# Optimization experiments

Measured on AMD Instinct MI355X. Metric: run time of the kernel, lower is better.

The kernel has to match this reference:

```python
import jax, jax.numpy as jnp
import numpy as np

K = 8192
D = 512
BETA = 0.25


def setup_inputs() -> dict:
    key = jax.random.key(0)
    k_z, k_cb = jax.random.split(key)
    z = jax.random.normal(k_z, (8, 4096, D), dtype=jnp.float32)
    codebook = jax.random.normal(k_cb, (K, D), dtype=jnp.float32)
    return {"z": z, "codebook": codebook}


def reference(z, codebook):
    B, Q, Din = z.shape
    flat = z.reshape(-1, Din)                      # (N, D)
    x2 = jnp.sum(flat * flat, axis=1, keepdims=True)   # (N, 1)
    e2 = jnp.sum(codebook * codebook, axis=1)          # (K,)
    xe = flat @ codebook.T                             # (N, K)
    distances = x2 - 2.0 * xe + e2[None, :]
    indices = jnp.argmin(distances, axis=1)            # (N,)
    z_q = codebook[indices].reshape(B, Q, Din)

    codebook_loss = jnp.mean((z_q - jax.lax.stop_gradient(z)) ** 2)
    commitment_loss = jnp.mean((z - jax.lax.stop_gradient(z_q)) ** 2)
    vq_loss = codebook_loss + BETA * commitment_loss
    z_q_ste = z + jax.lax.stop_gradient(z_q - z)

    # perplexity from one-hot usage counts of this batch
    N = flat.shape[0]
    counts = jnp.zeros((codebook.shape[0],), dtype=jnp.float32).at[indices].add(1.0)
    probs = counts / jnp.asarray(N, dtype=jnp.float32)
    perplexity = jnp.exp(-jnp.sum(probs * jnp.log(probs + 1e-10)))

    return z_q_ste, vq_loss, indices.reshape(B, Q), perplexity
```

## Files before the change

kernel.cpp:

```cpp
#include <hip/hip_runtime.h>
#include <hip/hip_bf16.h>

#define K_CODES 8192
#define DIM     512
#define N_VEC   32768
#define MARGIN  0.35f
#define MARGIN2 0.02f

typedef __attribute__((ext_vector_type(8))) short   short8;
typedef __attribute__((ext_vector_type(8))) unsigned short ushort8;
typedef __attribute__((ext_vector_type(4))) float   float4x;

__device__ inline void gl_lds16(const void* g, void* l) {
    __builtin_amdgcn_global_load_lds(
        (const __attribute__((address_space(1))) unsigned int*)g,
        (__attribute__((address_space(3))) unsigned int*)l, 16, 0, 0);
}

__device__ inline unsigned short f2bf(float f, float* back) {
    unsigned int u = __float_as_uint(f);
    unsigned int r = (u + 0x7FFFu + ((u >> 16) & 1u)) >> 16;
    *back = __uint_as_float(r << 16);
    return (unsigned short)r;
}

__global__ __launch_bounds__(256) void vq_prep(
    const float* __restrict__ z, const float* __restrict__ cb,
    float* __restrict__ x2, float* __restrict__ hne2,
    unsigned short* __restrict__ zh, unsigned short* __restrict__ zl,
    unsigned short* __restrict__ ch, unsigned short* __restrict__ cl) {
    int wave = threadIdx.x >> 6;
    int lane = threadIdx.x & 63;
    int row  = blockIdx.x * 4 + wave;
    bool isZ = row < N_VEC;
    int lr = isZ ? row : row - N_VEC;
    const float* src = isZ ? z + (size_t)row * DIM : cb + (size_t)lr * DIM;

    const float4* s4 = (const float4*)src;
    float4 v0 = s4[lane * 2];
    float4 v1 = s4[lane * 2 + 1];
    float f[8] = {v0.x, v0.y, v0.z, v0.w, v1.x, v1.y, v1.z, v1.w};

    float s = 0.0f;
    ushort8 h8, l8;
#pragma unroll
    for (int i = 0; i < 8; ++i) {
        s += f[i] * f[i];
        float back, dummy;
        h8[i] = f2bf(f[i], &back);
        l8[i] = f2bf(f[i] - back, &dummy);
    }
    ((ushort8*)(isZ ? zh : ch))[(size_t)lr * 64 + lane] = h8;
    ((ushort8*)(isZ ? zl : cl))[(size_t)lr * 64 + lane] = l8;

#pragma unroll
    for (int off = 32; off >= 1; off >>= 1) s += __shfl_xor(s, off, 64);
    if (lane == 0) {
        if (isZ) x2[lr] = s;
        else     hne2[lr] = -0.5f * s;
    }
}

__global__ __launch_bounds__(256, 2) void vq_gemm(
    const unsigned short* __restrict__ zh, const unsigned short* __restrict__ ch,
    const float* __restrict__ hne2,
    float* __restrict__ pG, int* __restrict__ pN, float* __restrict__ pG2) {
    __shared__ short8 AsC[1024];
    __shared__ short8 BsC[2048];

    const int tid  = threadIdx.x;
    const int w    = tid >> 6;
    const int lane = tid & 63;
    const int wM   = w & 1;
    const int wN   = w >> 1;
    const int rowBase   = blockIdx.x * 128;
    const int half      = blockIdx.y;
    const int codeBase0 = half * 4096;

    const int low3 = lane & 7, m15 = lane & 15, hi4 = lane >> 4;

    unsigned aOff[4];
#pragma unroll
    for (int i = 0; i < 4; ++i) {
        int cell = (w * 4 + i) * 64 + lane;
        int r = cell >> 3, qs = cell & 7, q = qs ^ (r & 7);
        aOff[i] = ((unsigned)(rowBase + r) * DIM + q * 8) * 2;
    }
    unsigned bOff[8];
#pragma unroll
    for (int i = 0; i < 8; ++i) {
        int cell = (w * 8 + i) * 64 + lane;
        int c = cell >> 3, qs = cell & 7, q = qs ^ (c & 7);
        bOff[i] = ((unsigned)c * DIM + q * 8) * 2;
    }

    int rIdx[4], cIdx[8];
#pragma unroll
    for (int mf = 0; mf < 4; ++mf) rIdx[mf] = (wM * 64 + mf * 16 + m15) * 8;
#pragma unroll
    for (int nf = 0; nf < 8; ++nf) cIdx[nf] = (wN * 128 + nf * 16 + m15) * 8;

    float g1[4][4], g2[4][4];
    int   n1[4][4];
#pragma unroll
    for (int mf = 0; mf < 4; ++mf)
#pragma unroll
        for (int rg = 0; rg < 4; ++rg) {
            g1[mf][rg] = -3.4e38f; g2[mf][rg] = -3.4e38f; n1[mf][rg] = 0;
        }

    const char* pA = (const char*)zh;
    for (int ct = 0; ct < 16; ++ct) {
        const int codeBase = codeBase0 + ct * 256;
        const char* pB = (const char*)ch + (size_t)codeBase * (DIM * 2);
        float4x acc[4][8];
#pragma unroll
        for (int mf = 0; mf < 4; ++mf)
#pragma unroll
            for (int nf = 0; nf < 8; ++nf) acc[mf][nf] = (float4x){0.f, 0.f, 0.f, 0.f};

        for (int dc = 0; dc < DIM; dc += 64) {
            const int dc2 = dc * 2;
            __syncthreads();
#pragma unroll
            for (int i = 0; i < 4; ++i)
                gl_lds16(pA + aOff[i] + dc2, &AsC[(w * 4 + i) * 64]);
#pragma unroll
            for (int i = 0; i < 8; ++i)
                gl_lds16(pB + bOff[i] + dc2, &BsC[(w * 8 + i) * 64]);
            __syncthreads();

#pragma unroll
            for (int ks = 0; ks < 2; ++ks) {
                const int qx = (ks * 4 + hi4) ^ low3;
                short8 a[4];
#pragma unroll
                for (int mf = 0; mf < 4; ++mf) a[mf] = AsC[rIdx[mf] + qx];
#pragma unroll
                for (int nf = 0; nf < 8; ++nf) {
                    short8 b = BsC[cIdx[nf] + qx];
#pragma unroll
                    for (int mf = 0; mf < 4; ++mf)
                        acc[mf][nf] = __builtin_amdgcn_mfma_f32_16x16x32_bf16(
                            a[mf], b, acc[mf][nf], 0, 0, 0);
                }
            }
        }

#pragma unroll
        for (int nf = 0; nf < 8; ++nf) {
            int nb = codeBase + wN * 128 + nf * 16 + m15;
            float hv = hne2[nb];
#pragma unroll
            for (int mf = 0; mf < 4; ++mf) {
#pragma unroll
                for (int rg = 0; rg < 4; ++rg) {
                    float g = acc[mf][nf][rg] + hv;
                    if (g > g1[mf][rg]) {
                        g2[mf][rg] = g1[mf][rg];
                        g1[mf][rg] = g; n1[mf][rg] = nb;
                    } else {
                        g2[mf][rg] = fmaxf(g2[mf][rg], g);
                    }
                }
            }
        }
    }

#pragma unroll
    for (int mf = 0; mf < 4; ++mf)
#pragma unroll
        for (int rg = 0; rg < 4; ++rg) {
            float a1 = g1[mf][rg], a2 = g2[mf][rg];
            int   an = n1[mf][rg];
#pragma unroll
            for (int off = 1; off <= 8; off <<= 1) {
                float b1 = __shfl_xor(a1, off, 64);
                int   bn = __shfl_xor(an, off, 64);
                float b2 = __shfl_xor(a2, off, 64);
                if (b1 > a1 || (b1 == a1 && bn < an)) {
                    a2 = fmaxf(a1, b2); a1 = b1; an = bn;
                } else {
                    a2 = fmaxf(a2, b1);
                }
            }
            if (m15 == 0) {
                int row  = rowBase + wM * 64 + mf * 16 + hi4 * 4 + rg;
                int slot = half * 2 + wN;
                pG [slot * N_VEC + row] = a1;
                pN [slot * N_VEC + row] = an;
                pG2[slot * N_VEC + row] = a2;
            }
        }
}

__global__ __launch_bounds__(256) void vq_scan(
    float* __restrict__ pG, const int* __restrict__ pN,
    const float* __restrict__ pG2,
    int* __restrict__ provIdx, int* __restrict__ flags,
    unsigned long long* __restrict__ keys,
    int* __restrict__ rescueRows, int* __restrict__ rescueCnt) {
    int r = blockIdx.x * 256 + threadIdx.x;
    float g1 = pG[r], g2 = pG2[r];
    int   n1 = pN[r];
#pragma unroll
    for (int s = 1; s < 4; ++s) {
        float a1 = pG [s * N_VEC + r];
        int   an = pN [s * N_VEC + r];
        float a2 = pG2[s * N_VEC + r];
        if (a1 > g1 || (a1 == g1 && an < n1)) {
            g2 = fmaxf(g1, a2); g1 = a1; n1 = an;
        } else {
            g2 = fmaxf(g2, a1);
        }
    }
    provIdx[r] = n1;
    pG[r] = g1;
    int fl = (g1 - g2 < MARGIN) ? 1 : 0;
    flags[r] = fl;
    if (fl) {
        keys[r] = ~0ull;
        int p = atomicAdd(rescueCnt, 1);
        rescueRows[p] = r;
    }
}

__global__ __launch_bounds__(256, 2) void vq_mid(
    const unsigned short* __restrict__ zh, const unsigned short* __restrict__ zl,
    const unsigned short* __restrict__ ch, const unsigned short* __restrict__ cl,
    const float* __restrict__ hne2,
    const int* __restrict__ rescueRows, const int* __restrict__ rescueCnt,
    float* __restrict__ pGm, int* __restrict__ pNm, float* __restrict__ pG2m) {
    __shared__ short8 AsC[512];
    __shared__ short8 BsC[2048];
    __shared__ int rowOf[64];

    const int tid  = threadIdx.x;
    const int w    = tid >> 6;
    const int lane = tid & 63;
    const int wM   = w & 1;
    const int wN   = w >> 1;
    const int cnt  = *rescueCnt;
    const int codeBase0 = blockIdx.y * 1024;

    const int low3 = lane & 7, m15 = lane & 15, hi4 = lane >> 4;

    unsigned bOff[8];
#pragma unroll
    for (int i = 0; i < 8; ++i) {
        int cell = (w * 8 + i) * 64 + lane;
        int c = cell >> 3, qs = cell & 7, q = qs ^ (c & 7);
        bOff[i] = ((unsigned)c * DIM + q * 8) * 2;
    }
    int aCellR[2], aCellQ[2];
#pragma unroll
    for (int i = 0; i < 2; ++i) {
        int cell = (w * 2 + i) * 64 + lane;
        aCellR[i] = cell >> 3;
        aCellQ[i] = (cell & 7) ^ (aCellR[i] & 7);
    }

    int rIdx[2], cIdx[8];
#pragma unroll
    for (int mf = 0; mf < 2; ++mf) rIdx[mf] = (wM * 32 + mf * 16 + m15) * 8;
#pragma unroll
    for (int nf = 0; nf < 8; ++nf) cIdx[nf] = (wN * 128 + nf * 16 + m15) * 8;

    for (int rt = blockIdx.x; rt * 64 < cnt; rt += gridDim.x) {
        __syncthreads();
        if (tid < 64) rowOf[tid] = rescueRows[rt * 64 + tid];
        __syncthreads();

        unsigned aOff[2];
#pragma unroll
        for (int i = 0; i < 2; ++i)
            aOff[i] = ((unsigned)rowOf[aCellR[i]] * DIM + aCellQ[i] * 8) * 2;

        float g1[2][4], g2[2][4];
        int   n1[2][4];
#pragma unroll
        for (int mf = 0; mf < 2; ++mf)
#pragma unroll
            for (int rg = 0; rg < 4; ++rg) {
                g1[mf][rg] = -3.4e38f; g2[mf][rg] = -3.4e38f; n1[mf][rg] = 0;
            }

        for (int ct = 0; ct < 4; ++ct) {
            const int codeBase = codeBase0 + ct * 256;
            float4x acc[2][8];
#pragma unroll
            for (int mf = 0; mf < 2; ++mf)
#pragma unroll
                for (int nf = 0; nf < 8; ++nf) acc[mf][nf] = (float4x){0.f, 0.f, 0.f, 0.f};

#pragma unroll
            for (int pass = 0; pass < 3; ++pass) {
                const char* pA = (const char*)(pass == 1 ? zl : zh);
                const char* pB = (const char*)(pass == 2 ? cl : ch)
                                 + (size_t)codeBase * (DIM * 2);
                for (int dc = 0; dc < DIM; dc += 64) {
                    const int dc2 = dc * 2;
                    __syncthreads();
#pragma unroll
                    for (int i = 0; i < 2; ++i)
                        gl_lds16(pA + aOff[i] + dc2, &AsC[(w * 2 + i) * 64]);
#pragma unroll
                    for (int i = 0; i < 8; ++i)
                        gl_lds16(pB + bOff[i] + dc2, &BsC[(w * 8 + i) * 64]);
                    __syncthreads();

#pragma unroll
                    for (int ks = 0; ks < 2; ++ks) {
                        const int qx = (ks * 4 + hi4) ^ low3;
                        short8 a[2];
#pragma unroll
                        for (int mf = 0; mf < 2; ++mf) a[mf] = AsC[rIdx[mf] + qx];
#pragma unroll
                        for (int nf = 0; nf < 8; ++nf) {
                            short8 b = BsC[cIdx[nf] + qx];
#pragma unroll
                            for (int mf = 0; mf < 2; ++mf)
                                acc[mf][nf] = __builtin_amdgcn_mfma_f32_16x16x32_bf16(
                                    a[mf], b, acc[mf][nf], 0, 0, 0);
                        }
                    }
                }
            }

#pragma unroll
            for (int nf = 0; nf < 8; ++nf) {
                int nb = codeBase + wN * 128 + nf * 16 + m15;
                float hv = hne2[nb];
#pragma unroll
                for (int mf = 0; mf < 2; ++mf) {
#pragma unroll
                    for (int rg = 0; rg < 4; ++rg) {
                        float g = acc[mf][nf][rg] + hv;
                        if (g > g1[mf][rg]) {
                            g2[mf][rg] = g1[mf][rg];
                            g1[mf][rg] = g; n1[mf][rg] = nb;
                        } else {
                            g2[mf][rg] = fmaxf(g2[mf][rg], g);
                        }
                    }
                }
            }
        }

#pragma unroll
        for (int mf = 0; mf < 2; ++mf)
#pragma unroll
            for (int rg = 0; rg < 4; ++rg) {
                float a1 = g1[mf][rg], a2 = g2[mf][rg];
                int   an = n1[mf][rg];
#pragma unroll
                for (int off = 1; off <= 8; off <<= 1) {
                    float b1 = __shfl_xor(a1, off, 64);
                    int   bn = __shfl_xor(an, off, 64);
                    float b2 = __shfl_xor(a2, off, 64);
                    if (b1 > a1 || (b1 == a1 && bn < an)) {
                        a2 = fmaxf(a1, b2); a1 = b1; an = bn;
                    } else {
                        a2 = fmaxf(a2, b1);
                    }
                }
                if (m15 == 0) {
                    int sPos = rt * 64 + wM * 32 + mf * 16 + hi4 * 4 + rg;
                    int slot = blockIdx.y * 2 + wN;
                    pGm [slot * N_VEC + sPos] = a1;
                    pNm [slot * N_VEC + sPos] = an;
                    pG2m[slot * N_VEC + sPos] = a2;
                }
            }
    }
}

__global__ __launch_bounds__(256) void vq_scan2(
    const float* __restrict__ pGm, const int* __restrict__ pNm,
    const float* __restrict__ pG2m,
    const int* __restrict__ rescueRows, const int* __restrict__ rescueCnt,
    unsigned long long* __restrict__ keys,
    int* __restrict__ rescueRows2, int* __restrict__ rescueCnt2) {
    int s = blockIdx.x * 256 + threadIdx.x;
    if (s >= *rescueCnt) return;
    float g1 = pGm[s], g2 = pG2m[s];
    int   n1 = pNm[s];
#pragma unroll
    for (int k = 1; k < 16; ++k) {
        float a1 = pGm [k * N_VEC + s];
        int   an = pNm [k * N_VEC + s];
        float a2 = pG2m[k * N_VEC + s];
        if (a1 > g1 || (a1 == g1 && an < n1)) {
            g2 = fmaxf(g1, a2); g1 = a1; n1 = an;
        } else {
            g2 = fmaxf(g2, a1);
        }
    }
    int row = rescueRows[s];
    if (g1 - g2 < MARGIN2) {
        keys[row] = ~0ull;
        int p = atomicAdd(rescueCnt2, 1);
        rescueRows2[p] = row;
    } else {
        keys[row] = ((unsigned long long)__float_as_uint(-g1) << 32) |
                    (unsigned long long)(unsigned)n1;
    }
}

#define RBM 64
#define RBK 256
#define RBD 32

__global__ __launch_bounds__(256, 2) void vq_exact(
    const float* __restrict__ z, const float* __restrict__ cb,
    const float* __restrict__ hne2,
    const int* __restrict__ rescueRows2, const int* __restrict__ rescueCnt2,
    unsigned long long* __restrict__ keys) {
    __shared__ float As[RBD][RBM];
    __shared__ float Bs[RBD][RBK];
    __shared__ int   rowOf[RBM];

    const int tid = threadIdx.x;
    const int tx  = tid & 31;
    const int ty  = tid >> 5;
    const int cnt = *rescueCnt2;
    const int codeBase0 = blockIdx.y * 512;
    const int sw = (tx & 8) ? 4 : 0;
    const int sRow = tid >> 2;
    const int sQ   = tid & 3;

    for (int rt = blockIdx.x; rt * RBM < cnt; rt += gridDim.x) {
        const int slotBase = rt * RBM;
        __syncthreads();
        if (tid < RBM) rowOf[tid] = rescueRows2[slotBase + tid];
        __syncthreads();

        float best[8];
        int   bidx[8];
#pragma unroll
        for (int i = 0; i < 8; ++i) { best[i] = 3.4e38f; bidx[i] = K_CODES; }

        for (int kt = 0; kt < 2; ++kt) {
            const int codeBase = codeBase0 + kt * RBK;
            float acc[8][8];
#pragma unroll
            for (int i = 0; i < 8; ++i)
#pragma unroll
                for (int j = 0; j < 8; ++j) acc[i][j] = 0.0f;

            for (int dc = 0; dc < DIM; dc += RBD) {
                __syncthreads();
                {
                    const float* srcA = z + (size_t)rowOf[sRow] * DIM + dc + sQ * 8;
                    float4 va0 = ((const float4*)srcA)[0];
                    float4 va1 = ((const float4*)srcA)[1];
                    int c0 = sQ * 8;
                    As[c0 + 0][sRow] = va0.x; As[c0 + 1][sRow] = va0.y;
                    As[c0 + 2][sRow] = va0.z; As[c0 + 3][sRow] = va0.w;
                    As[c0 + 4][sRow] = va1.x; As[c0 + 5][sRow] = va1.y;
                    As[c0 + 6][sRow] = va1.z; As[c0 + 7][sRow] = va1.w;
                }
                {
                    const float4* srcB = (const float4*)(cb + (size_t)(codeBase + tid) * DIM + dc);
#pragma unroll
                    for (int j = 0; j < 8; ++j) {
                        float4 v = srcB[j];
                        Bs[j * 4 + 0][tid] = v.x; Bs[j * 4 + 1][tid] = v.y;
                        Bs[j * 4 + 2][tid] = v.z; Bs[j * 4 + 3][tid] = v.w;
                    }
                }
                __syncthreads();

#pragma unroll
                for (int d = 0; d < RBD; ++d) {
                    float a[8], b[8];
                    *(float4*)&a[0] = *(const float4*)&As[d][ty * 8];
                    *(float4*)&a[4] = *(const float4*)&As[d][ty * 8 + 4];
                    *(float4*)&b[0] = *(const float4*)&Bs[d][tx * 8 + sw];
                    *(float4*)&b[4] = *(const float4*)&Bs[d][tx * 8 + (sw ^ 4)];
#pragma unroll
                    for (int i = 0; i < 8; ++i)
#pragma unroll
                        for (int j = 0; j < 8; ++j) acc[i][j] += a[i] * b[j];
                }
            }

#pragma unroll
            for (int j = 0; j < 8; ++j) {
                int code = codeBase + tx * 8 + ((j < 4) ? (sw + j) : ((sw ^ 4) + j - 4));
                float ev = -hne2[code];
#pragma unroll
                for (int i = 0; i < 8; ++i) {
                    float kv = ev - acc[i][j];
                    if (kv < best[i] || (kv == best[i] && code < bidx[i])) {
                        best[i] = kv;
                        bidx[i] = code;
                    }
                }
            }
        }

#pragma unroll
        for (int off = 16; off >= 1; off >>= 1) {
#pragma unroll
            for (int i = 0; i < 8; ++i) {
                float od = __shfl_xor(best[i], off, 64);
                int   oi = __shfl_xor(bidx[i], off, 64);
                if (od < best[i] || (od == best[i] && oi < bidx[i])) {
                    best[i] = od;
                    bidx[i] = oi;
                }
            }
        }

        if (tx == 0) {
#pragma unroll
            for (int i = 0; i < 8; ++i) {
                int slot = slotBase + ty * 8 + i;
                if (slot < cnt) {
                    unsigned long long key =
                        ((unsigned long long)__float_as_uint(best[i]) << 32) |
                        (unsigned long long)(unsigned)bidx[i];
                    atomicMin(&keys[rowOf[ty * 8 + i]], key);
                }
            }
        }
    }
}

__global__ __launch_bounds__(256) void vq_final(
    const float* __restrict__ gBest, const int* __restrict__ provIdx,
    const int* __restrict__ flags, const unsigned long long* __restrict__ keys,
    const float* __restrict__ x2, const float* __restrict__ cb,
    float* __restrict__ zq, float* __restrict__ idxf,
    float* __restrict__ counts, float* __restrict__ lossAcc) {
    __shared__ int   sIdx[256];
    __shared__ float wsum[4];
    const int tid = threadIdx.x;
    const int r   = blockIdx.x * 256 + tid;

    int n; float dist;
    if (flags[r]) {
        unsigned long long k = keys[r];
        n = (int)(unsigned)(k & 0xffffffffu);
        float kv = __uint_as_float((unsigned)(k >> 32));
        dist = x2[r] + 2.0f * kv;
    } else {
        n = provIdx[r];
        dist = x2[r] - 2.0f * gBest[r];
    }
    sIdx[tid] = n;
    idxf[r]   = (float)n;
    atomicAdd(&counts[n], 1.0f);

    float ls = dist;
#pragma unroll
    for (int off = 32; off >= 1; off >>= 1) ls += __shfl_xor(ls, off, 64);
    if ((tid & 63) == 0) wsum[tid >> 6] = ls;
    __syncthreads();
    if (tid == 0) atomicAdd(lossAcc, wsum[0] + wsum[1] + wsum[2] + wsum[3]);

    const float4* cb4 = (const float4*)cb;
    float4* zq4 = (float4*)(zq + (size_t)blockIdx.x * 256 * DIM);
    for (int t = tid; t < 256 * (DIM / 4); t += 256) {
        int row = t >> 7, f4 = t & 127;
        zq4[(size_t)row * 128 + f4] = cb4[(size_t)sIdx[row] * 128 + f4];
    }
}

__global__ __launch_bounds__(256) void vq_finalize(const float* __restrict__ counts,
                                                   const float* __restrict__ lossAcc,
                                                   float* __restrict__ out_loss,
                                                   float* __restrict__ out_perp) {
    __shared__ float wsum[4];
    int tid = threadIdx.x;
    float s = 0.0f;
    for (int i = tid; i < K_CODES; i += 256) {
        float p = counts[i] * (1.0f / (float)N_VEC);
        s += p * logf(p + 1e-10f);
    }
#pragma unroll
    for (int off = 32; off >= 1; off >>= 1) s += __shfl_xor(s, off, 64);
    if ((tid & 63) == 0) wsum[tid >> 6] = s;
    __syncthreads();
    if (tid == 0) {
        *out_perp = expf(-(wsum[0] + wsum[1] + wsum[2] + wsum[3]));
        *out_loss = 1.25f * lossAcc[0] / (float)(N_VEC * DIM);
    }
}

extern "C" void kernel_launch(void* const* d_in, const int* in_sizes, int n_in,
                              void* d_out, int out_size, void* d_ws, size_t ws_size,
                              hipStream_t stream) {
    (void)in_sizes; (void)n_in; (void)out_size; (void)ws_size;
    const float* z  = (const float*)d_in[0];
    const float* cb = (const float*)d_in[1];

    char* ws = (char*)d_ws;
    float* x2         = (float*)(ws + 0);
    float* hne2       = (float*)(ws + 131072);
    float* counts     = (float*)(ws + 163840);
    float* lossAcc    = (float*)(ws + 196608);
    int*   rescueCnt  = (int*)  (ws + 196612);
    int*   rescueCnt2 = (int*)  (ws + 196616);
    int*   provIdx    = (int*)  (ws + 262144);
    int*   flags      = (int*)  (ws + 393216);
    unsigned long long* keys = (unsigned long long*)(ws + 524288);
    int*   rescueRows  = (int*)(ws + 786432);
    int*   rescueRows2 = (int*)(ws + 917504);
    float* pG         = (float*)(ws + 1048576);
    int*   pN         = (int*)  (ws + 1572864);
    float* pG2        = (float*)(ws + 2097152);
    float* pGm        = (float*)(ws + 2621440);
    int*   pNm        = (int*)  (ws + 4718592);
    float* pG2m       = (float*)(ws + 6815744);
    unsigned short* zh = (unsigned short*)(ws + 8912896);
    unsigned short* zl = (unsigned short*)(ws + 42467328);
    unsigned short* ch = (unsigned short*)(ws + 76021760);
    unsigned short* cl = (unsigned short*)(ws + 84410368);

    float* out      = (float*)d_out;
    float* zq       = out;
    float* out_loss = out + 16777216;
    float* idxf     = out + 16777217;
    float* out_perp = out + 16777217 + 32768;

    hipMemsetAsync(counts, 0, 32768 + 12, stream);
    hipMemsetAsync(rescueRows, 0, 262144, stream);
    vq_prep<<<(N_VEC + K_CODES) / 4, 256, 0, stream>>>(z, cb, x2, hne2, zh, zl, ch, cl);
    dim3 grid(N_VEC / 128, 2);
    vq_gemm<<<grid, 256, 0, stream>>>(zh, ch, hne2, pG, pN, pG2);
    vq_scan<<<N_VEC / 256, 256, 0, stream>>>(pG, pN, pG2, provIdx, flags, keys,
                                             rescueRows, rescueCnt);
    dim3 mgrid(32, 8);
    vq_mid<<<mgrid, 256, 0, stream>>>(zh, zl, ch, cl, hne2, rescueRows, rescueCnt,
                                      pGm, pNm, pG2m);
    vq_scan2<<<N_VEC / 256, 256, 0, stream>>>(pGm, pNm, pG2m, rescueRows, rescueCnt,
                                              keys, rescueRows2, rescueCnt2);
    dim3 egrid(8, 16);
    vq_exact<<<egrid, 256, 0, stream>>>(z, cb, hne2, rescueRows2, rescueCnt2, keys);
    vq_final<<<N_VEC / 256, 256, 0, stream>>>(pG, provIdx, flags, keys, x2, cb,
                                              zq, idxf, counts, lossAcc);
    vq_finalize<<<1, 256, 0, stream>>>(counts, lossAcc, out_loss, out_perp);
}
```

Baseline: 728.0 us.

## Retile rescue GEMM to 128-row by 256-code tiles and cap rescue count

```diff
diff --git a/kernel.cpp b/kernel.cpp
--- a/kernel.cpp
+++ b/kernel.cpp
@@ -6,6 +6,7 @@
 #define N_VEC   32768
 #define MARGIN  0.35f
 #define MARGIN2 0.02f
+#define MAXC    8192
 
 typedef __attribute__((ext_vector_type(8))) short   short8;
 typedef __attribute__((ext_vector_type(8))) unsigned short ushort8;
@@ -199,7 +200,8 @@
     const float* __restrict__ pG2,
     int* __restrict__ provIdx, int* __restrict__ flags,
     unsigned long long* __restrict__ keys,
-    int* __restrict__ rescueRows, int* __restrict__ rescueCnt) {
+    int* __restrict__ rescueRows, int* __restrict__ rescueCnt,
+    int* __restrict__ rescueRows2, int* __restrict__ rescueCnt2) {
     int r = blockIdx.x * 256 + threadIdx.x;
     float g1 = pG[r], g2 = pG2[r];
     int   n1 = pN[r];
@@ -221,7 +223,12 @@
     if (fl) {
         keys[r] = ~0ull;
         int p = atomicAdd(rescueCnt, 1);
-        rescueRows[p] = r;
+        if (p < MAXC) {
+            rescueRows[p] = r;
+        } else {
+            int q = atomicAdd(rescueCnt2, 1);
+            rescueRows2[q] = r;
+        }
     }
 }
 
@@ -231,124 +238,119 @@
     const float* __restrict__ hne2,
     const int* __restrict__ rescueRows, const int* __restrict__ rescueCnt,
     float* __restrict__ pGm, int* __restrict__ pNm, float* __restrict__ pG2m) {
-    __shared__ short8 AsC[512];
+    __shared__ short8 AsC[1024];
     __shared__ short8 BsC[2048];
-    __shared__ int rowOf[64];
+    __shared__ int rowOf[128];
 
     const int tid  = threadIdx.x;
     const int w    = tid >> 6;
     const int lane = tid & 63;
     const int wM   = w & 1;
     const int wN   = w >> 1;
-    const int cnt  = *rescueCnt;
-    const int codeBase0 = blockIdx.y * 1024;
+    int cnt = *rescueCnt; if (cnt > MAXC) cnt = MAXC;
+    const int rowTiles = (cnt + 127) >> 7;
+    const int codeBase = blockIdx.y * 256;
 
     const int low3 = lane & 7, m15 = lane & 15, hi4 = lane >> 4;
 
+    int aCellR[4], aCellQ[4];
+#pragma unroll
+    for (int i = 0; i < 4; ++i) {
+        int cell = (w * 4 + i) * 64 + lane;
+        aCellR[i] = cell >> 3;
+        aCellQ[i] = (cell & 7) ^ (aCellR[i] & 7);
+    }
     unsigned bOff[8];
 #pragma unroll
     for (int i = 0; i < 8; ++i) {
         int cell = (w * 8 + i) * 64 + lane;
         int c = cell >> 3, qs = cell & 7, q = qs ^ (c & 7);
-        bOff[i] = ((unsigned)c * DIM + q * 8) * 2;
-    }
-    int aCellR[2], aCellQ[2];
-#pragma unroll
-    for (int i = 0; i < 2; ++i) {
-        int cell = (w * 2 + i) * 64 + lane;
-        aCellR[i] = cell >> 3;
-        aCellQ[i] = (cell & 7) ^ (aCellR[i] & 7);
-    }
-
-    int rIdx[2], cIdx[8];
-#pragma unroll
-    for (int mf = 0; mf < 2; ++mf) rIdx[mf] = (wM * 32 + mf * 16 + m15) * 8;
+        bOff[i] = ((unsigned)(codeBase + c) * DIM + q * 8) * 2;
+    }
+
+    int rIdx[4], cIdx[8];
+#pragma unroll
+    for (int mf = 0; mf < 4; ++mf) rIdx[mf] = (wM * 64 + mf * 16 + m15) * 8;
 #pragma unroll
     for (int nf = 0; nf < 8; ++nf) cIdx[nf] = (wN * 128 + nf * 16 + m15) * 8;
 
-    for (int rt = blockIdx.x; rt * 64 < cnt; rt += gridDim.x) {
+    for (int rt = blockIdx.x; rt < rowTiles; rt += gridDim.x) {
         __syncthreads();
-        if (tid < 64) rowOf[tid] = rescueRows[rt * 64 + tid];
+        if (tid < 128) rowOf[tid] = rescueRows[rt * 128 + tid];
         __syncthreads();
 
-        unsigned aOff[2];
-#pragma unroll
-        for (int i = 0; i < 2; ++i)
+        unsigned aOff[4];
+#pragma unroll
+        for (int i = 0; i < 4; ++i)
             aOff[i] = ((unsigned)rowOf[aCellR[i]] * DIM + aCellQ[i] * 8) * 2;
 
-        float g1[2][4], g2[2][4];
-        int   n1[2][4];
-#pragma unroll
-        for (int mf = 0; mf < 2; ++mf)
+        float4x acc[4][8];
+#pragma unroll
+        for (int mf = 0; mf < 4; ++mf)
+#pragma unroll
+            for (int nf = 0; nf < 8; ++nf) acc[mf][nf] = (float4x){0.f, 0.f, 0.f, 0.f};
+
+#pragma unroll
+        for (int pass = 0; pass < 3; ++pass) {
+            const char* pA = (const char*)(pass == 1 ? zl : zh);
+            const char* pB = (const char*)(pass == 2 ? cl : ch);
+            for (int dc = 0; dc < DIM; dc += 64) {
+                const int dc2 = dc * 2;
+                __syncthreads();
+#pragma unroll
+                for (int i = 0; i < 4; ++i)
+                    gl_lds16(pA + aOff[i] + dc2, &AsC[(w * 4 + i) * 64]);
+#pragma unroll
+                for (int i = 0; i < 8; ++i)
+                    gl_lds16(pB + bOff[i] + dc2, &BsC[(w * 8 + i) * 64]);
+                __syncthreads();
+
+#pragma unroll
+                for (int ks = 0; ks < 2; ++ks) {
+                    const int qx = (ks * 4 + hi4) ^ low3;
+                    short8 a[4];
+#pragma unroll
+                    for (int mf = 0; mf < 4; ++mf) a[mf] = AsC[rIdx[mf] + qx];
+#pragma unroll
+                    for (int nf = 0; nf < 8; ++nf) {
+                        short8 b = BsC[cIdx[nf] + qx];
+#pragma unroll
+                        for (int mf = 0; mf < 4; ++mf)
+                            acc[mf][nf] = __builtin_amdgcn_mfma_f32_16x16x32_bf16(
+                                a[mf], b, acc[mf][nf], 0, 0, 0);
+                    }
+                }
+            }
+        }
+
+        float g1[4][4], g2[4][4];
+        int   n1[4][4];
+#pragma unroll
+        for (int mf = 0; mf < 4; ++mf)
 #pragma unroll
             for (int rg = 0; rg < 4; ++rg) {
                 g1[mf][rg] = -3.4e38f; g2[mf][rg] = -3.4e38f; n1[mf][rg] = 0;
             }
-
-        for (int ct = 0; ct < 4; ++ct) {
-            const int codeBase = codeBase0 + ct * 256;
-            float4x acc[2][8];
-#pragma unroll
-            for (int mf = 0; mf < 2; ++mf)
-#pragma unroll
-                for (int nf = 0; nf < 8; ++nf) acc[mf][nf] = (float4x){0.f, 0.f, 0.f, 0.f};
-
-#pragma unroll
-            for (int pass = 0; pass < 3; ++pass) {
-                const char* pA = (const char*)(pass == 1 ? zl : zh);
-                const char* pB = (const char*)(pass == 2 ? cl : ch)
-                                 + (size_t)codeBase * (DIM * 2);
-                for (int dc = 0; dc < DIM; dc += 64) {
-                    const int dc2 = dc * 2;
-                    __syncthreads();
-#pragma unroll
-                    for (int i = 0; i < 2; ++i)
-                        gl_lds16(pA + aOff[i] + dc2, &AsC[(w * 2 + i) * 64]);
-#pragma unroll
-                    for (int i = 0; i < 8; ++i)
-                        gl_lds16(pB + bOff[i] + dc2, &BsC[(w * 8 + i) * 64]);
-                    __syncthreads();
-
-#pragma unroll
-                    for (int ks = 0; ks < 2; ++ks) {
-                        const int qx = (ks * 4 + hi4) ^ low3;
-                        short8 a[2];
-#pragma unroll
-                        for (int mf = 0; mf < 2; ++mf) a[mf] = AsC[rIdx[mf] + qx];
-#pragma unroll
-                        for (int nf = 0; nf < 8; ++nf) {
-                            short8 b = BsC[cIdx[nf] + qx];
-#pragma unroll
-                            for (int mf = 0; mf < 2; ++mf)
-                                acc[mf][nf] = __builtin_amdgcn_mfma_f32_16x16x32_bf16(
-                                    a[mf], b, acc[mf][nf], 0, 0, 0);
-                        }
+#pragma unroll
+        for (int nf = 0; nf < 8; ++nf) {
+            int nb = codeBase + wN * 128 + nf * 16 + m15;
+            float hv = hne2[nb];
+#pragma unroll
+            for (int mf = 0; mf < 4; ++mf) {
+#pragma unroll
+                for (int rg = 0; rg < 4; ++rg) {
+                    float g = acc[mf][nf][rg] + hv;
+                    if (g > g1[mf][rg]) {
+                        g2[mf][rg] = g1[mf][rg];
+                        g1[mf][rg] = g; n1[mf][rg] = nb;
+                    } else {
+                        g2[mf][rg] = fmaxf(g2[mf][rg], g);
                     }
                 }
             }
-
-#pragma unroll
-            for (int nf = 0; nf < 8; ++nf) {
-                int nb = codeBase + wN * 128 + nf * 16 + m15;
-                float hv = hne2[nb];
-#pragma unroll
-                for (int mf = 0; mf < 2; ++mf) {
-#pragma unroll
-                    for (int rg = 0; rg < 4; ++rg) {
-                        float g = acc[mf][nf][rg] + hv;
-                        if (g > g1[mf][rg]) {
-                            g2[mf][rg] = g1[mf][rg];
-                            g1[mf][rg] = g; n1[mf][rg] = nb;
-                        } else {
-                            g2[mf][rg] = fmaxf(g2[mf][rg], g);
-                        }
-                    }
-                }
-            }
-        }
-
-#pragma unroll
-        for (int mf = 0; mf < 2; ++mf)
+        }
+#pragma unroll
+        for (int mf = 0; mf < 4; ++mf)
 #pragma unroll
             for (int rg = 0; rg < 4; ++rg) {
                 float a1 = g1[mf][rg], a2 = g2[mf][rg];
@@ -365,11 +367,11 @@
                     }
                 }
                 if (m15 == 0) {
-                    int sPos = rt * 64 + wM * 32 + mf * 16 + hi4 * 4 + rg;
+                    int sPos = rt * 128 + wM * 64 + mf * 16 + hi4 * 4 + rg;
                     int slot = blockIdx.y * 2 + wN;
-                    pGm [slot * N_VEC + sPos] = a1;
-                    pNm [slot * N_VEC + sPos] = an;
-                    pG2m[slot * N_VEC + sPos] = a2;
+                    pGm [slot * MAXC + sPos] = a1;
+                    pNm [slot * MAXC + sPos] = an;
+                    pG2m[slot * MAXC + sPos] = a2;
                 }
             }
     }
@@ -382,14 +384,15 @@
     unsigned long long* __restrict__ keys,
     int* __restrict__ rescueRows2, int* __restrict__ rescueCnt2) {
     int s = blockIdx.x * 256 + threadIdx.x;
-    if (s >= *rescueCnt) return;
+    int cnt = *rescueCnt; if (cnt > MAXC) cnt = MAXC;
+    if (s >= cnt) return;
     float g1 = pGm[s], g2 = pG2m[s];
     int   n1 = pNm[s];
-#pragma unroll
-    for (int k = 1; k < 16; ++k) {
-        float a1 = pGm [k * N_VEC + s];
-        int   an = pNm [k * N_VEC + s];
-        float a2 = pG2m[k * N_VEC + s];
+#pragma unroll 8
+    for (int k = 1; k < 64; ++k) {
+        float a1 = pGm [k * MAXC + s];
+        int   an = pNm [k * MAXC + s];
+        float a2 = pG2m[k * MAXC + s];
         if (a1 > g1 || (a1 == g1 && an < n1)) {
             g2 = fmaxf(g1, a2); g1 = a1; n1 = an;
         } else {
@@ -631,12 +634,13 @@
     dim3 grid(N_VEC / 128, 2);
     vq_gemm<<<grid, 256, 0, stream>>>(zh, ch, hne2, pG, pN, pG2);
     vq_scan<<<N_VEC / 256, 256, 0, stream>>>(pG, pN, pG2, provIdx, flags, keys,
-                                             rescueRows, rescueCnt);
-    dim3 mgrid(32, 8);
+                                             rescueRows, rescueCnt,
+                                             rescueRows2, rescueCnt2);
+    dim3 mgrid(16, 32);
     vq_mid<<<mgrid, 256, 0, stream>>>(zh, zl, ch, cl, hne2, rescueRows, rescueCnt,
                                       pGm, pNm, pG2m);
-    vq_scan2<<<N_VEC / 256, 256, 0, stream>>>(pGm, pNm, pG2m, rescueRows, rescueCnt,
-                                              keys, rescueRows2, rescueCnt2);
+    vq_scan2<<<MAXC / 256, 256, 0, stream>>>(pGm, pNm, pG2m, rescueRows, rescueCnt,
+                                             keys, rescueRows2, rescueCnt2);
     dim3 egrid(8, 16);
     vq_exact<<<egrid, 256, 0, stream>>>(z, cb, hne2, rescueRows2, rescueCnt2, keys);
     vq_final<<<N_VEC / 256, 256, 0, stream>>>(pG, provIdx, flags, keys, x2, cb,
```

New measurement: 686.8 us. 1.06x faster.

## Flatten rescue GEMM work into row-tile by code-strip units with capped rescue list

Applied to the files above, without the earlier changes.

```diff
diff --git a/kernel.cpp b/kernel.cpp
--- a/kernel.cpp
+++ b/kernel.cpp
@@ -6,6 +6,7 @@
 #define N_VEC   32768
 #define MARGIN  0.35f
 #define MARGIN2 0.02f
+#define MAXC    8192
 
 typedef __attribute__((ext_vector_type(8))) short   short8;
 typedef __attribute__((ext_vector_type(8))) unsigned short ushort8;
@@ -199,7 +200,8 @@
     const float* __restrict__ pG2,
     int* __restrict__ provIdx, int* __restrict__ flags,
     unsigned long long* __restrict__ keys,
-    int* __restrict__ rescueRows, int* __restrict__ rescueCnt) {
+    int* __restrict__ rescueRows, int* __restrict__ rescueCnt,
+    int* __restrict__ rescueRows2, int* __restrict__ rescueCnt2) {
     int r = blockIdx.x * 256 + threadIdx.x;
     float g1 = pG[r], g2 = pG2[r];
     int   n1 = pN[r];
@@ -221,11 +223,16 @@
     if (fl) {
         keys[r] = ~0ull;
         int p = atomicAdd(rescueCnt, 1);
-        rescueRows[p] = r;
-    }
-}
-
-__global__ __launch_bounds__(256, 2) void vq_mid(
+        if (p < MAXC) {
+            rescueRows[p] = r;
+        } else {
+            int q = atomicAdd(rescueCnt2, 1);
+            rescueRows2[q] = r;
+        }
+    }
+}
+
+__global__ __launch_bounds__(256, 3) void vq_mid(
     const unsigned short* __restrict__ zh, const unsigned short* __restrict__ zl,
     const unsigned short* __restrict__ ch, const unsigned short* __restrict__ cl,
     const float* __restrict__ hne2,
@@ -240,11 +247,18 @@
     const int lane = tid & 63;
     const int wM   = w & 1;
     const int wN   = w >> 1;
-    const int cnt  = *rescueCnt;
-    const int codeBase0 = blockIdx.y * 1024;
+    int cnt = *rescueCnt; if (cnt > MAXC) cnt = MAXC;
+    const int nUnits = ((cnt + 63) >> 6) * 32;
 
     const int low3 = lane & 7, m15 = lane & 15, hi4 = lane >> 4;
 
+    int aCellR[2], aCellQ[2];
+#pragma unroll
+    for (int i = 0; i < 2; ++i) {
+        int cell = (w * 2 + i) * 64 + lane;
+        aCellR[i] = cell >> 3;
+        aCellQ[i] = (cell & 7) ^ (aCellR[i] & 7);
+    }
     unsigned bOff[8];
 #pragma unroll
     for (int i = 0; i < 8; ++i) {
@@ -252,13 +266,6 @@
         int c = cell >> 3, qs = cell & 7, q = qs ^ (c & 7);
         bOff[i] = ((unsigned)c * DIM + q * 8) * 2;
     }
-    int aCellR[2], aCellQ[2];
-#pragma unroll
-    for (int i = 0; i < 2; ++i) {
-        int cell = (w * 2 + i) * 64 + lane;
-        aCellR[i] = cell >> 3;
-        aCellQ[i] = (cell & 7) ^ (aCellR[i] & 7);
-    }
 
     int rIdx[2], cIdx[8];
 #pragma unroll
@@ -266,7 +273,11 @@
 #pragma unroll
     for (int nf = 0; nf < 8; ++nf) cIdx[nf] = (wN * 128 + nf * 16 + m15) * 8;
 
-    for (int rt = blockIdx.x; rt * 64 < cnt; rt += gridDim.x) {
+    for (int u = blockIdx.x; u < nUnits; u += gridDim.x) {
+        const int rt    = u >> 5;
+        const int strip = u & 31;
+        const int codeBase = strip * 256;
+
         __syncthreads();
         if (tid < 64) rowOf[tid] = rescueRows[rt * 64 + tid];
         __syncthreads();
@@ -276,6 +287,46 @@
         for (int i = 0; i < 2; ++i)
             aOff[i] = ((unsigned)rowOf[aCellR[i]] * DIM + aCellQ[i] * 8) * 2;
 
+        float4x acc[2][8];
+#pragma unroll
+        for (int mf = 0; mf < 2; ++mf)
+#pragma unroll
+            for (int nf = 0; nf < 8; ++nf) acc[mf][nf] = (float4x){0.f, 0.f, 0.f, 0.f};
+
+#pragma unroll
+        for (int pass = 0; pass < 3; ++pass) {
+            const char* pA = (const char*)(pass == 1 ? zl : zh);
+            const char* pB = (const char*)(pass == 2 ? cl : ch)
+                             + (size_t)codeBase * (DIM * 2);
+            for (int dc = 0; dc < DIM; dc += 64) {
+                const int dc2 = dc * 2;
+                __syncthreads();
+#pragma unroll
+                for (int i = 0; i < 2; ++i)
+                    gl_lds16(pA + aOff[i] + dc2, &AsC[(w * 2 + i) * 64]);
+#pragma unroll
+                for (int i = 0; i < 8; ++i)
+                    gl_lds16(pB + bOff[i] + dc2, &BsC[(w * 8 + i) * 64]);
+                __syncthreads();
+
+#pragma unroll
+                for (int ks = 0; ks < 2; ++ks) {
+                    const int qx = (ks * 4 + hi4) ^ low3;
+                    short8 a[2];
+#pragma unroll
+                    for (int mf = 0; mf < 2; ++mf) a[mf] = AsC[rIdx[mf] + qx];
+#pragma unroll
+                    for (int nf = 0; nf < 8; ++nf) {
+                        short8 b = BsC[cIdx[nf] + qx];
+#pragma unroll
+                        for (int mf = 0; mf < 2; ++mf)
+                            acc[mf][nf] = __builtin_amdgcn_mfma_f32_16x16x32_bf16(
+                                a[mf], b, acc[mf][nf], 0, 0, 0);
+                    }
+                }
+            }
+        }
+
         float g1[2][4], g2[2][4];
         int   n1[2][4];
 #pragma unroll
@@ -284,69 +335,24 @@
             for (int rg = 0; rg < 4; ++rg) {
                 g1[mf][rg] = -3.4e38f; g2[mf][rg] = -3.4e38f; n1[mf][rg] = 0;
             }
-
-        for (int ct = 0; ct < 4; ++ct) {
-            const int codeBase = codeBase0 + ct * 256;
-            float4x acc[2][8];
-#pragma unroll
-            for (int mf = 0; mf < 2; ++mf)
-#pragma unroll
-                for (int nf = 0; nf < 8; ++nf) acc[mf][nf] = (float4x){0.f, 0.f, 0.f, 0.f};
-
-#pragma unroll
-            for (int pass = 0; pass < 3; ++pass) {
-                const char* pA = (const char*)(pass == 1 ? zl : zh);
-                const char* pB = (const char*)(pass == 2 ? cl : ch)
-                                 + (size_t)codeBase * (DIM * 2);
-                for (int dc = 0; dc < DIM; dc += 64) {
-                    const int dc2 = dc * 2;
-                    __syncthreads();
-#pragma unroll
-                    for (int i = 0; i < 2; ++i)
-                        gl_lds16(pA + aOff[i] + dc2, &AsC[(w * 2 + i) * 64]);
-#pragma unroll
-                    for (int i = 0; i < 8; ++i)
-                        gl_lds16(pB + bOff[i] + dc2, &BsC[(w * 8 + i) * 64]);
-                    __syncthreads();
-
-#pragma unroll
-                    for (int ks = 0; ks < 2; ++ks) {
-                        const int qx = (ks * 4 + hi4) ^ low3;
-                        short8 a[2];
-#pragma unroll
-                        for (int mf = 0; mf < 2; ++mf) a[mf] = AsC[rIdx[mf] + qx];
-#pragma unroll
-                        for (int nf = 0; nf < 8; ++nf) {
-                            short8 b = BsC[cIdx[nf] + qx];
-#pragma unroll
-                            for (int mf = 0; mf < 2; ++mf)
-                                acc[mf][nf] = __builtin_amdgcn_mfma_f32_16x16x32_bf16(
-                                    a[mf], b, acc[mf][nf], 0, 0, 0);
-                        }
+#pragma unroll
+        for (int nf = 0; nf < 8; ++nf) {
+            int nb = codeBase + wN * 128 + nf * 16 + m15;
+            float hv = hne2[nb];
+#pragma unroll
+            for (int mf = 0; mf < 2; ++mf) {
+#pragma unroll
+                for (int rg = 0; rg < 4; ++rg) {
+                    float g = acc[mf][nf][rg] + hv;
+                    if (g > g1[mf][rg]) {
+                        g2[mf][rg] = g1[mf][rg];
+                        g1[mf][rg] = g; n1[mf][rg] = nb;
+                    } else {
+                        g2[mf][rg] = fmaxf(g2[mf][rg], g);
                     }
                 }
             }
-
-#pragma unroll
-            for (int nf = 0; nf < 8; ++nf) {
-                int nb = codeBase + wN * 128 + nf * 16 + m15;
-                float hv = hne2[nb];
-#pragma unroll
-                for (int mf = 0; mf < 2; ++mf) {
-#pragma unroll
-                    for (int rg = 0; rg < 4; ++rg) {
-                        float g = acc[mf][nf][rg] + hv;
-                        if (g > g1[mf][rg]) {
-                            g2[mf][rg] = g1[mf][rg];
-                            g1[mf][rg] = g; n1[mf][rg] = nb;
-                        } else {
-                            g2[mf][rg] = fmaxf(g2[mf][rg], g);
-                        }
-                    }
-                }
-            }
-        }
-
+        }
 #pragma unroll
         for (int mf = 0; mf < 2; ++mf)
 #pragma unroll
@@ -366,10 +372,10 @@
                 }
                 if (m15 == 0) {
                     int sPos = rt * 64 + wM * 32 + mf * 16 + hi4 * 4 + rg;
-                    int slot = blockIdx.y * 2 + wN;
-                    pGm [slot * N_VEC + sPos] = a1;
-                    pNm [slot * N_VEC + sPos] = an;
-                    pG2m[slot * N_VEC + sPos] = a2;
+                    int slot = strip * 2 + wN;
+                    pGm [slot * MAXC + sPos] = a1;
+                    pNm [slot * MAXC + sPos] = an;
+                    pG2m[slot * MAXC + sPos] = a2;
                 }
             }
     }
@@ -382,14 +388,15 @@
     unsigned long long* __restrict__ keys,
     int* __restrict__ rescueRows2, int* __restrict__ rescueCnt2) {
     int s = blockIdx.x * 256 + threadIdx.x;
-    if (s >= *rescueCnt) return;
+    int cnt = *rescueCnt; if (cnt > MAXC) cnt = MAXC;
+    if (s >= cnt) return;
     float g1 = pGm[s], g2 = pG2m[s];
     int   n1 = pNm[s];
-#pragma unroll
-    for (int k = 1; k < 16; ++k) {
-        float a1 = pGm [k * N_VEC + s];
-        int   an = pNm [k * N_VEC + s];
-        float a2 = pG2m[k * N_VEC + s];
+#pragma unroll 8
+    for (int k = 1; k < 64; ++k) {
+        float a1 = pGm [k * MAXC + s];
+        int   an = pNm [k * MAXC + s];
+        float a2 = pG2m[k * MAXC + s];
         if (a1 > g1 || (a1 == g1 && an < n1)) {
             g2 = fmaxf(g1, a2); g1 = a1; n1 = an;
         } else {
@@ -424,7 +431,7 @@
     const int tx  = tid & 31;
     const int ty  = tid >> 5;
     const int cnt = *rescueCnt2;
-    const int codeBase0 = blockIdx.y * 512;
+    const int codeBase = blockIdx.y * RBK;
     const int sw = (tx & 8) ? 4 : 0;
     const int sRow = tid >> 2;
     const int sQ   = tid & 3;
@@ -440,62 +447,59 @@
 #pragma unroll
         for (int i = 0; i < 8; ++i) { best[i] = 3.4e38f; bidx[i] = K_CODES; }
 
-        for (int kt = 0; kt < 2; ++kt) {
-            const int codeBase = codeBase0 + kt * RBK;
-            float acc[8][8];
-#pragma unroll
-            for (int i = 0; i < 8; ++i)
-#pragma unroll
-                for (int j = 0; j < 8; ++j) acc[i][j] = 0.0f;
-
-            for (int dc = 0; dc < DIM; dc += RBD) {
-                __syncthreads();
-                {
-                    const float* srcA = z + (size_t)rowOf[sRow] * DIM + dc + sQ * 8;
-                    float4 va0 = ((const float4*)srcA)[0];
-                    float4 va1 = ((const float4*)srcA)[1];
-                    int c0 = sQ * 8;
-                    As[c0 + 0][sRow] = va0.x; As[c0 + 1][sRow] = va0.y;
-                    As[c0 + 2][sRow] = va0.z; As[c0 + 3][sRow] = va0.w;
-                    As[c0 + 4][sRow] = va1.x; As[c0 + 5][sRow] = va1.y;
-                    As[c0 + 6][sRow] = va1.z; As[c0 + 7][sRow] = va1.w;
-                }
-                {
-                    const float4* srcB = (const float4*)(cb + (size_t)(codeBase + tid) * DIM + dc);
-#pragma unroll
-                    for (int j = 0; j < 8; ++j) {
-                        float4 v = srcB[j];
-                        Bs[j * 4 + 0][tid] = v.x; Bs[j * 4 + 1][tid] = v.y;
-                        Bs[j * 4 + 2][tid] = v.z; Bs[j * 4 + 3][tid] = v.w;
-                    }
-                }
-                __syncthreads();
-
-#pragma unroll
-                for (int d = 0; d < RBD; ++d) {
-                    float a[8], b[8];
-                    *(float4*)&a[0] = *(const float4*)&As[d][ty * 8];
-                    *(float4*)&a[4] = *(const float4*)&As[d][ty * 8 + 4];
-                    *(float4*)&b[0] = *(const float4*)&Bs[d][tx * 8 + sw];
-                    *(float4*)&b[4] = *(const float4*)&Bs[d][tx * 8 + (sw ^ 4)];
-#pragma unroll
-                    for (int i = 0; i < 8; ++i)
-#pragma unroll
-                        for (int j = 0; j < 8; ++j) acc[i][j] += a[i] * b[j];
-                }
-            }
-
-#pragma unroll
-            for (int j = 0; j < 8; ++j) {
-                int code = codeBase + tx * 8 + ((j < 4) ? (sw + j) : ((sw ^ 4) + j - 4));
-                float ev = -hne2[code];
-#pragma unroll
-                for (int i = 0; i < 8; ++i) {
-                    float kv = ev - acc[i][j];
-                    if (kv < best[i] || (kv == best[i] && code < bidx[i])) {
-                        best[i] = kv;
-                        bidx[i] = code;
-                    }
+        float acc[8][8];
+#pragma unroll
+        for (int i = 0; i < 8; ++i)
+#pragma unroll
+            for (int j = 0; j < 8; ++j) acc[i][j] = 0.0f;
+
+        for (int dc = 0; dc < DIM; dc += RBD) {
+            __syncthreads();
+            {
+                const float* srcA = z + (size_t)rowOf[sRow] * DIM + dc + sQ * 8;
+                float4 va0 = ((const float4*)srcA)[0];
+                float4 va1 = ((const float4*)srcA)[1];
+                int c0 = sQ * 8;
+                As[c0 + 0][sRow] = va0.x; As[c0 + 1][sRow] = va0.y;
+                As[c0 + 2][sRow] = va0.z; As[c0 + 3][sRow] = va0.w;
+                As[c0 + 4][sRow] = va1.x; As[c0 + 5][sRow] = va1.y;
+                As[c0 + 6][sRow] = va1.z; As[c0 + 7][sRow] = va1.w;
+            }
+            {
+                const float4* srcB = (const float4*)(cb + (size_t)(codeBase + tid) * DIM + dc);
+#pragma unroll
+                for (int j = 0; j < 8; ++j) {
+                    float4 v = srcB[j];
+                    Bs[j * 4 + 0][tid] = v.x; Bs[j * 4 + 1][tid] = v.y;
+                    Bs[j * 4 + 2][tid] = v.z; Bs[j * 4 + 3][tid] = v.w;
+                }
+            }
+            __syncthreads();
+
+#pragma unroll
+            for (int d = 0; d < RBD; ++d) {
+                float a[8], b[8];
+                *(float4*)&a[0] = *(const float4*)&As[d][ty * 8];
+                *(float4*)&a[4] = *(const float4*)&As[d][ty * 8 + 4];
+                *(float4*)&b[0] = *(const float4*)&Bs[d][tx * 8 + sw];
+                *(float4*)&b[4] = *(const float4*)&Bs[d][tx * 8 + (sw ^ 4)];
+#pragma unroll
+                for (int i = 0; i < 8; ++i)
+#pragma unroll
+                    for (int j = 0; j < 8; ++j) acc[i][j] += a[i] * b[j];
+            }
+        }
+
+#pragma unroll
+        for (int j = 0; j < 8; ++j) {
+            int code = codeBase + tx * 8 + ((j < 4) ? (sw + j) : ((sw ^ 4) + j - 4));
+            float ev = -hne2[code];
+#pragma unroll
+            for (int i = 0; i < 8; ++i) {
+                float kv = ev - acc[i][j];
+                if (kv < best[i] || (kv == best[i] && code < bidx[i])) {
+                    best[i] = kv;
+                    bidx[i] = code;
                 }
             }
         }
@@ -631,13 +635,13 @@
     dim3 grid(N_VEC / 128, 2);
     vq_gemm<<<grid, 256, 0, stream>>>(zh, ch, hne2, pG, pN, pG2);
     vq_scan<<<N_VEC / 256, 256, 0, stream>>>(pG, pN, pG2, provIdx, flags, keys,
-                                             rescueRows, rescueCnt);
-    dim3 mgrid(32, 8);
-    vq_mid<<<mgrid, 256, 0, stream>>>(zh, zl, ch, cl, hne2, rescueRows, rescueCnt,
-                                      pGm, pNm, pG2m);
-    vq_scan2<<<N_VEC / 256, 256, 0, stream>>>(pGm, pNm, pG2m, rescueRows, rescueCnt,
-                                              keys, rescueRows2, rescueCnt2);
-    dim3 egrid(8, 16);
+                                             rescueRows, rescueCnt,
+                                             rescueRows2, rescueCnt2);
+    vq_mid<<<768, 256, 0, stream>>>(zh, zl, ch, cl, hne2, rescueRows, rescueCnt,
+                                    pGm, pNm, pG2m);
+    vq_scan2<<<MAXC / 256, 256, 0, stream>>>(pGm, pNm, pG2m, rescueRows, rescueCnt,
+                                             keys, rescueRows2, rescueCnt2);
+    dim3 egrid(4, 32);
     vq_exact<<<egrid, 256, 0, stream>>>(z, cb, hne2, rescueRows2, rescueCnt2, keys);
     vq_final<<<N_VEC / 256, 256, 0, stream>>>(pG, provIdx, flags, keys, x2, cb,
                                               zq, idxf, counts, lossAcc);
```

Measured after the change: 700.4 us. 3.8% less time.
